# Kernel tuning notes

Hardware: AMD Instinct MI355X
Metric: run time of the kernel (lower is better)

## Reference

```python
import jax, jax.numpy as jnp
import numpy as np

N, K, DIM = 50000, 16, 256
SLOPE = 0.2

def _leaky(x):
    return jnp.where(x >= 0, x, SLOPE * x)

def _mlp(x, w, b):
    # torch nn.Linear followed by LeakyReLU(0.2); w is [in, out]
    return _leaky(x @ w + b)

def setup_inputs() -> dict:
    key = jax.random.key(0)
    ks = jax.random.split(key, 14)
    d4, d2 = DIM // 4, DIM // 2
    def lin(k, i, o):
        kw, kb = jax.random.split(k)
        s = 1.0 / np.sqrt(i)
        return (jax.random.uniform(kw, (i, o), jnp.float32, -s, s),
                jax.random.uniform(kb, (o,), jnp.float32, -s, s))
    w_res, b_res = lin(ks[0], DIM, DIM)
    w_init, b_init = lin(ks[1], DIM, d4)
    w_g1, b_g1 = lin(ks[2], 4, d4)
    w_g2, b_g2 = lin(ks[3], 4, d2)
    w_fin, b_fin = lin(ks[4], DIM, DIM)
    return {
        "input_features": jax.random.normal(ks[5], (N, DIM), jnp.float32),
        "geom_features": jax.random.normal(ks[6], (N, K, 4), jnp.float32),
        "closest_indices": jax.random.randint(ks[7], (N, K), 0, N, jnp.int32),
        "w_res": w_res, "b_res": b_res,
        "w_init": w_init, "b_init": b_init,
        "w_g1": w_g1, "b_g1": b_g1,
        "w_g2": w_g2, "b_g2": b_g2,
        "w_fin": w_fin, "b_fin": b_fin,
    }

def _lfa(feat, geom, idx, w_g, b_g):
    # feat: [N, d]; geom: [N, K, 4]; idx: [N, K]
    g = _mlp(geom, w_g, b_g)                 # [N, K, d]
    gathered = feat[idx]                      # [N, K, d] gather over points
    combined = jnp.concatenate([g, gathered], axis=-1)  # [N, K, 2d]
    return jnp.mean(combined, axis=1)         # [N, 2d]

def reference(input_features, geom_features, closest_indices,
              w_res, b_res, w_init, b_init, w_g1, b_g1, w_g2, b_g2,
              w_fin, b_fin):
    residual = _mlp(input_features, w_res, b_res)            # [N, DIM]
    a = _mlp(input_features, w_init, b_init)                 # [N, DIM/4]
    a = _lfa(a, geom_features, closest_indices, w_g1, b_g1)  # [N, DIM/2]
    a = _lfa(a, geom_features, closest_indices, w_g2, b_g2)  # [N, DIM]
    a = _mlp(a, w_fin, b_fin)                                # [N, DIM]
    return a + residual
```

## Files before the change

### kernel.cpp

```cpp
#include <hip/hip_runtime.h>

#define DIM 256
#define KNN 16
#define SLOPE 0.2f

typedef unsigned short u16;
typedef __attribute__((ext_vector_type(8))) unsigned short u16x8;
typedef __attribute__((ext_vector_type(4))) unsigned short u16x4;
typedef __attribute__((ext_vector_type(8))) short s16x8;
typedef __attribute__((ext_vector_type(4))) float f32x4;

__device__ __forceinline__ float leaky(float x) { return x >= 0.f ? x : SLOPE * x; }
__device__ __forceinline__ u16 f2bu(float f) {
    unsigned int u = __float_as_uint(f);
    u = (u + 0x7FFFu + ((u >> 16) & 1u)) >> 16;
    return (u16)u;
}
__device__ __forceinline__ float bu2f(u16 h) {
    return __uint_as_float(((unsigned int)h) << 16);
}

__global__ __launch_bounds__(256) void k_prep(
    const float* __restrict__ w_res, const float* __restrict__ w_init,
    const float* __restrict__ w_fin, u16* __restrict__ wT1, u16* __restrict__ wT3)
{
    const int t = blockIdx.x * 256 + threadIdx.x;
    if (t < 20 * 8 * 64) {
        const int lane = t & 63, frag = t >> 6;
        const int ks = frag & 7, ct = frag >> 3;
        const int col = ct * 16 + (lane & 15);
        const int k0 = ks * 32 + (lane >> 4) * 8;
        u16x8 p;
        #pragma unroll
        for (int j = 0; j < 8; ++j) {
            float v = (col < 256) ? w_res[(size_t)(k0 + j) * 256 + col]
                                  : w_init[(size_t)(k0 + j) * 64 + (col - 256)];
            p[j] = f2bu(v);
        }
        *(u16x8*)(wT1 + (size_t)t * 8) = p;
    } else if (t < 20 * 8 * 64 + 16 * 8 * 64) {
        const int u = t - 20 * 8 * 64;
        const int lane = u & 63, frag = u >> 6;
        const int ks = frag & 7, ct = frag >> 3;
        const int col = ct * 16 + (lane & 15);
        const int k0 = ks * 32 + (lane >> 4) * 8;
        u16x8 p;
        #pragma unroll
        for (int j = 0; j < 8; ++j)
            p[j] = f2bu(w_fin[(size_t)(k0 + j) * 256 + col]);
        *(u16x8*)(wT3 + (size_t)u * 8) = p;
    }
}

#define APAD 264
__global__ __launch_bounds__(256) void k_gemm1(
    const float* __restrict__ in, const u16* __restrict__ wT1,
    const float* __restrict__ b_res, const float* __restrict__ b_init,
    float* __restrict__ resid, u16* __restrict__ a1, int N)
{
    __shared__ u16 A_s[64 * APAD];
    const int t = threadIdx.x;
    const int base = blockIdx.x * 64;

    {
        const int row = t >> 2, seg = t & 3;
        const int grow = min(base + row, N - 1);
        const float* src = in + (size_t)grow * DIM + seg * 64;
        u16* dst = &A_s[row * APAD + seg * 64];
        #pragma unroll
        for (int j = 0; j < 8; ++j) {
            float4 f0 = *(const float4*)(src + j * 8);
            float4 f1 = *(const float4*)(src + j * 8 + 4);
            u16x8 p;
            p[0] = f2bu(f0.x); p[1] = f2bu(f0.y); p[2] = f2bu(f0.z); p[3] = f2bu(f0.w);
            p[4] = f2bu(f1.x); p[5] = f2bu(f1.y); p[6] = f2bu(f1.z); p[7] = f2bu(f1.w);
            *(u16x8*)(dst + j * 8) = p;
        }
    }
    __syncthreads();

    f32x4 acc[4][5];
    #pragma unroll
    for (int i = 0; i < 4; ++i)
        #pragma unroll
        for (int j = 0; j < 5; ++j)
            acc[i][j] = (f32x4){0.f, 0.f, 0.f, 0.f};

    const int w = t >> 6, lane = t & 63;
    const int llow = lane & 15, lhi = lane >> 4;

    for (int ks = 0; ks < 8; ++ks) {
        s16x8 bfrag[5];
        #pragma unroll
        for (int ci = 0; ci < 5; ++ci) {
            const int ct = w * 5 + ci;
            bfrag[ci] = *(const s16x8*)(wT1 + ((size_t)(ct * 8 + ks) * 64 + lane) * 8);
        }
        s16x8 afrag[4];
        #pragma unroll
        for (int rt = 0; rt < 4; ++rt)
            afrag[rt] = *(const s16x8*)(&A_s[(rt * 16 + llow) * APAD + ks * 32 + lhi * 8]);
        #pragma unroll
        for (int ci = 0; ci < 5; ++ci)
            #pragma unroll
            for (int rt = 0; rt < 4; ++rt)
                acc[rt][ci] = __builtin_amdgcn_mfma_f32_16x16x32_bf16(
                    afrag[rt], bfrag[ci], acc[rt][ci], 0, 0, 0);
    }

    #pragma unroll
    for (int ci = 0; ci < 5; ++ci) {
        const int ct = w * 5 + ci;
        const int col = ct * 16 + llow;
        if (col < 256) {
            const float bias = b_res[col];
            #pragma unroll
            for (int rt = 0; rt < 4; ++rt)
                #pragma unroll
                for (int r = 0; r < 4; ++r) {
                    int row = base + rt * 16 + lhi * 4 + r;
                    if (row < N)
                        resid[(size_t)row * DIM + col] = leaky(acc[rt][ci][r] + bias);
                }
        } else {
            const int c2 = col - 256;
            const float bias = b_init[c2];
            #pragma unroll
            for (int rt = 0; rt < 4; ++rt)
                #pragma unroll
                for (int r = 0; r < 4; ++r) {
                    int row = base + rt * 16 + lhi * 4 + r;
                    if (row < N)
                        a1[(size_t)row * 64 + c2] = f2bu(leaky(acc[rt][ci][r] + bias));
                }
        }
    }
}

__global__ __launch_bounds__(256) void k_lfa1(
    const float* __restrict__ geom, const int* __restrict__ idx,
    const float* __restrict__ w_g1, const float* __restrict__ b_g1,
    const u16* __restrict__ a1, u16* __restrict__ a2, int N)
{
    __shared__ float geom_s[16 * KNN * 4];
    __shared__ int idx_s[16 * KNN];
    const int t = threadIdx.x;
    const int base = blockIdx.x * 16;

    {
        size_t off = (size_t)base * 64 + t * 4;
        size_t mx = (size_t)N * 64 - 4;
        if (off > mx) off = mx;
        *(float4*)&geom_s[t * 4] = *(const float4*)(geom + off);
        int io = base * KNN + t;
        if (t < 256) idx_s[t] = idx[min(io, N * KNN - 1)];
    }
    __syncthreads();

    const int pt = t >> 4, s = t & 15;
    const int n = base + pt;

    float wr[4][4], bb[4];
    #pragma unroll
    for (int r = 0; r < 4; ++r)
        #pragma unroll
        for (int j = 0; j < 4; ++j)
            wr[r][j] = w_g1[r * 64 + s * 4 + j];
    #pragma unroll
    for (int j = 0; j < 4; ++j) bb[j] = b_g1[s * 4 + j];

    float accM[4] = {0.f, 0.f, 0.f, 0.f};
    const float4* g4 = (const float4*)&geom_s[pt * 64];
    #pragma unroll
    for (int k = 0; k < KNN; ++k) {
        float4 g = g4[k];
        #pragma unroll
        for (int j = 0; j < 4; ++j)
            accM[j] += leaky(g.x * wr[0][j] + g.y * wr[1][j] + g.z * wr[2][j] + g.w * wr[3][j] + bb[j]);
    }

    float accG[4] = {0.f, 0.f, 0.f, 0.f};
    #pragma unroll
    for (int k = 0; k < KNN; ++k) {
        u16x4 u = *(const u16x4*)(a1 + (size_t)idx_s[pt * KNN + k] * 64 + s * 4);
        #pragma unroll
        for (int j = 0; j < 4; ++j) accG[j] += bu2f(u[j]);
    }

    if (n < N) {
        u16x4 pm, pg;
        #pragma unroll
        for (int j = 0; j < 4; ++j) {
            pm[j] = f2bu(accM[j] * 0.0625f);
            pg[j] = f2bu(accG[j] * 0.0625f);
        }
        *(u16x4*)(a2 + (size_t)n * 128 + s * 4) = pm;
        *(u16x4*)(a2 + (size_t)n * 128 + 64 + s * 4) = pg;
    }
}

__global__ __launch_bounds__(256) void k_lfa2_fin(
    const float* __restrict__ geom, const int* __restrict__ idx,
    const float* __restrict__ w_g2, const float* __restrict__ b_g2,
    const u16* __restrict__ a2, const u16* __restrict__ wT3,
    const float* __restrict__ b_fin, float* __restrict__ out, int N)
{
    __shared__ u16 a3_s[64 * APAD];
    __shared__ float geom_s[64 * KNN * 4];
    __shared__ int idx_s[64 * KNN];
    const int t = threadIdx.x;
    const int base = blockIdx.x * 64;

    {
        size_t mx = (size_t)N * 64 - 4;
        #pragma unroll
        for (int j = 0; j < 4; ++j) {
            size_t off = (size_t)base * 64 + t * 4 + j * 1024;
            if (off > mx) off = mx;
            *(float4*)&geom_s[t * 4 + j * 1024] = *(const float4*)(geom + off);
        }
        int imx = N * KNN - 1;
        #pragma unroll
        for (int j = 0; j < 4; ++j) {
            int off = base * KNN + t + j * 256;
            idx_s[t + j * 256] = idx[min(off, imx)];
        }
    }
    __syncthreads();

    {
        const int c = t & 127, h = t >> 7;
        const float w0 = w_g2[c], w1 = w_g2[128 + c], w2 = w_g2[256 + c],
                    w3 = w_g2[384 + c], bb = b_g2[c];
        for (int p = 0; p < 32; ++p) {
            const int pt = h * 32 + p;
            float acc = 0.f;
            const float4* g4 = (const float4*)&geom_s[pt * 64];
            #pragma unroll
            for (int k = 0; k < KNN; ++k) {
                float4 g = g4[k];
                acc += leaky(g.x * w0 + g.y * w1 + g.z * w2 + g.w * w3 + bb);
            }
            a3_s[pt * APAD + c] = f2bu(acc * 0.0625f);
        }
    }
    {
        const int pt = t >> 2, q = t & 3;
        float acc[32];
        #pragma unroll
        for (int j = 0; j < 32; ++j) acc[j] = 0.f;
        for (int k = 0; k < KNN; ++k) {
            const u16* row = a2 + (size_t)idx_s[pt * KNN + k] * 128 + q * 32;
            #pragma unroll
            for (int v = 0; v < 4; ++v) {
                u16x8 u = *(const u16x8*)(row + v * 8);
                #pragma unroll
                for (int j = 0; j < 8; ++j) acc[v * 8 + j] += bu2f(u[j]);
            }
        }
        #pragma unroll
        for (int v = 0; v < 4; ++v) {
            u16x8 p;
            #pragma unroll
            for (int j = 0; j < 8; ++j) p[j] = f2bu(acc[v * 8 + j] * 0.0625f);
            *(u16x8*)(&a3_s[pt * APAD + 128 + q * 32 + v * 8]) = p;
        }
    }
    __syncthreads();

    f32x4 acc[4][4];
    #pragma unroll
    for (int i = 0; i < 4; ++i)
        #pragma unroll
        for (int j = 0; j < 4; ++j)
            acc[i][j] = (f32x4){0.f, 0.f, 0.f, 0.f};

    const int w = t >> 6, lane = t & 63;
    const int llow = lane & 15, lhi = lane >> 4;

    for (int ks = 0; ks < 8; ++ks) {
        s16x8 bfrag[4];
        #pragma unroll
        for (int ci = 0; ci < 4; ++ci) {
            const int ct = w * 4 + ci;
            bfrag[ci] = *(const s16x8*)(wT3 + ((size_t)(ct * 8 + ks) * 64 + lane) * 8);
        }
        s16x8 afrag[4];
        #pragma unroll
        for (int rt = 0; rt < 4; ++rt)
            afrag[rt] = *(const s16x8*)(&a3_s[(rt * 16 + llow) * APAD + ks * 32 + lhi * 8]);
        #pragma unroll
        for (int ci = 0; ci < 4; ++ci)
            #pragma unroll
            for (int rt = 0; rt < 4; ++rt)
                acc[rt][ci] = __builtin_amdgcn_mfma_f32_16x16x32_bf16(
                    afrag[rt], bfrag[ci], acc[rt][ci], 0, 0, 0);
    }

    #pragma unroll
    for (int ci = 0; ci < 4; ++ci) {
        const int ct = w * 4 + ci;
        const int col = ct * 16 + llow;
        const float bias = b_fin[col];
        #pragma unroll
        for (int rt = 0; rt < 4; ++rt)
            #pragma unroll
            for (int r = 0; r < 4; ++r) {
                int row = base + rt * 16 + lhi * 4 + r;
                if (row < N) {
                    size_t o = (size_t)row * DIM + col;
                    out[o] = leaky(acc[rt][ci][r] + bias) + out[o];
                }
            }
    }
}

extern "C" void kernel_launch(void* const* d_in, const int* in_sizes, int n_in,
                              void* d_out, int out_size, void* d_ws, size_t ws_size,
                              hipStream_t stream) {
    const float* in    = (const float*)d_in[0];
    const float* geom  = (const float*)d_in[1];
    const int*   idx   = (const int*)d_in[2];
    const float* w_res = (const float*)d_in[3];
    const float* b_res = (const float*)d_in[4];
    const float* w_init= (const float*)d_in[5];
    const float* b_init= (const float*)d_in[6];
    const float* w_g1  = (const float*)d_in[7];
    const float* b_g1  = (const float*)d_in[8];
    const float* w_g2  = (const float*)d_in[9];
    const float* b_g2  = (const float*)d_in[10];
    const float* w_fin = (const float*)d_in[11];
    const float* b_fin = (const float*)d_in[12];
    float* out = (float*)d_out;

    const int N = in_sizes[0] / DIM;

    char* ws = (char*)d_ws;
    u16* a1  = (u16*)ws;
    u16* a2  = (u16*)(ws + (size_t)N * 64 * 2);
    u16* wT1 = (u16*)(ws + (size_t)N * (64 + 128) * 2);
    u16* wT3 = wT1 + 320 * 256;

    k_prep<<<72, 256, 0, stream>>>(w_res, w_init, w_fin, wT1, wT3);
    k_gemm1<<<(N + 63) / 64, 256, 0, stream>>>(in, wT1, b_res, b_init, out, a1, N);
    k_lfa1<<<(N + 15) / 16, 256, 0, stream>>>(geom, idx, w_g1, b_g1, a1, a2, N);
    k_lfa2_fin<<<(N + 63) / 64, 256, 0, stream>>>(geom, idx, w_g2, b_g2, a2, wT3, b_fin, out, N);
}
```

Before: 296.9 us.

## Split gemm1 accumulators into two passes and drop LDS staging in lfa2_fin

k_gemm1 now computes its five column tiles in two passes (3 then 2) with a shared epilogue helper, which shrinks the live accumulator set so that launch_bounds(256,4) can fit. k_lfa2_fin drops the geom and idx shared-memory staging and its barrier, reading geom directly from global memory and loading each point's indices as int4 vectors. Its gather loop now issues two neighbours' loads before accumulating, to keep more memory requests in flight. In exchange, the A fragments are reloaded from LDS in both gemm1 passes, and the geom reads in lfa2_fin are redundant across threads and may hit global or L2 repeatedly.

```diff
diff --git a/kernel.cpp b/kernel.cpp
--- a/kernel.cpp
+++ b/kernel.cpp
@@ -53,7 +53,38 @@
 }
 
 #define APAD 264
-__global__ __launch_bounds__(256) void k_gemm1(
+
+__device__ __forceinline__ void epi_gemm1(
+    int base, int N, int ct, int llow, int lhi, const f32x4* acc4,
+    const float* __restrict__ b_res, const float* __restrict__ b_init,
+    float* __restrict__ resid, u16* __restrict__ a1)
+{
+    const int col = ct * 16 + llow;
+    if (col < 256) {
+        const float bias = b_res[col];
+        #pragma unroll
+        for (int rt = 0; rt < 4; ++rt)
+            #pragma unroll
+            for (int r = 0; r < 4; ++r) {
+                int row = base + rt * 16 + lhi * 4 + r;
+                if (row < N)
+                    resid[(size_t)row * DIM + col] = leaky(acc4[rt][r] + bias);
+            }
+    } else {
+        const int c2 = col - 256;
+        const float bias = b_init[c2];
+        #pragma unroll
+        for (int rt = 0; rt < 4; ++rt)
+            #pragma unroll
+            for (int r = 0; r < 4; ++r) {
+                int row = base + rt * 16 + lhi * 4 + r;
+                if (row < N)
+                    a1[(size_t)row * 64 + c2] = f2bu(leaky(acc4[rt][r] + bias));
+            }
+    }
+}
+
+__global__ __launch_bounds__(256, 4) void k_gemm1(
     const float* __restrict__ in, const u16* __restrict__ wT1,
     const float* __restrict__ b_res, const float* __restrict__ b_init,
     float* __restrict__ resid, u16* __restrict__ a1, int N)
@@ -79,61 +110,66 @@
     }
     __syncthreads();
 
-    f32x4 acc[4][5];
-    #pragma unroll
-    for (int i = 0; i < 4; ++i)
-        #pragma unroll
-        for (int j = 0; j < 5; ++j)
-            acc[i][j] = (f32x4){0.f, 0.f, 0.f, 0.f};
-
     const int w = t >> 6, lane = t & 63;
     const int llow = lane & 15, lhi = lane >> 4;
 
-    for (int ks = 0; ks < 8; ++ks) {
-        s16x8 bfrag[5];
-        #pragma unroll
-        for (int ci = 0; ci < 5; ++ci) {
-            const int ct = w * 5 + ci;
-            bfrag[ci] = *(const s16x8*)(wT1 + ((size_t)(ct * 8 + ks) * 64 + lane) * 8);
-        }
-        s16x8 afrag[4];
-        #pragma unroll
-        for (int rt = 0; rt < 4; ++rt)
-            afrag[rt] = *(const s16x8*)(&A_s[(rt * 16 + llow) * APAD + ks * 32 + lhi * 8]);
-        #pragma unroll
-        for (int ci = 0; ci < 5; ++ci)
+    {
+        f32x4 acc[3][4];
+        #pragma unroll
+        for (int i = 0; i < 3; ++i)
+            #pragma unroll
+            for (int j = 0; j < 4; ++j)
+                acc[i][j] = (f32x4){0.f, 0.f, 0.f, 0.f};
+        for (int ks = 0; ks < 8; ++ks) {
+            s16x8 bfrag[3];
+            #pragma unroll
+            for (int ci = 0; ci < 3; ++ci) {
+                const int ct = w * 5 + ci;
+                bfrag[ci] = *(const s16x8*)(wT1 + ((size_t)(ct * 8 + ks) * 64 + lane) * 8);
+            }
+            s16x8 afrag[4];
             #pragma unroll
             for (int rt = 0; rt < 4; ++rt)
-                acc[rt][ci] = __builtin_amdgcn_mfma_f32_16x16x32_bf16(
-                    afrag[rt], bfrag[ci], acc[rt][ci], 0, 0, 0);
-    }
-
-    #pragma unroll
-    for (int ci = 0; ci < 5; ++ci) {
-        const int ct = w * 5 + ci;
-        const int col = ct * 16 + llow;
-        if (col < 256) {
-            const float bias = b_res[col];
+                afrag[rt] = *(const s16x8*)(&A_s[(rt * 16 + llow) * APAD + ks * 32 + lhi * 8]);
+            #pragma unroll
+            for (int ci = 0; ci < 3; ++ci)
+                #pragma unroll
+                for (int rt = 0; rt < 4; ++rt)
+                    acc[ci][rt] = __builtin_amdgcn_mfma_f32_16x16x32_bf16(
+                        afrag[rt], bfrag[ci], acc[ci][rt], 0, 0, 0);
+        }
+        #pragma unroll
+        for (int ci = 0; ci < 3; ++ci)
+            epi_gemm1(base, N, w * 5 + ci, llow, lhi, acc[ci], b_res, b_init, resid, a1);
+    }
+    {
+        f32x4 acc[2][4];
+        #pragma unroll
+        for (int i = 0; i < 2; ++i)
+            #pragma unroll
+            for (int j = 0; j < 4; ++j)
+                acc[i][j] = (f32x4){0.f, 0.f, 0.f, 0.f};
+        for (int ks = 0; ks < 8; ++ks) {
+            s16x8 bfrag[2];
+            #pragma unroll
+            for (int ci = 0; ci < 2; ++ci) {
+                const int ct = w * 5 + 3 + ci;
+                bfrag[ci] = *(const s16x8*)(wT1 + ((size_t)(ct * 8 + ks) * 64 + lane) * 8);
+            }
+            s16x8 afrag[4];
             #pragma unroll
             for (int rt = 0; rt < 4; ++rt)
+                afrag[rt] = *(const s16x8*)(&A_s[(rt * 16 + llow) * APAD + ks * 32 + lhi * 8]);
+            #pragma unroll
+            for (int ci = 0; ci < 2; ++ci)
                 #pragma unroll
-                for (int r = 0; r < 4; ++r) {
-                    int row = base + rt * 16 + lhi * 4 + r;
-                    if (row < N)
-                        resid[(size_t)row * DIM + col] = leaky(acc[rt][ci][r] + bias);
-                }
-        } else {
-            const int c2 = col - 256;
-            const float bias = b_init[c2];
-            #pragma unroll
-            for (int rt = 0; rt < 4; ++rt)
-                #pragma unroll
-                for (int r = 0; r < 4; ++r) {
-                    int row = base + rt * 16 + lhi * 4 + r;
-                    if (row < N)
-                        a1[(size_t)row * 64 + c2] = f2bu(leaky(acc[rt][ci][r] + bias));
-                }
-        }
+                for (int rt = 0; rt < 4; ++rt)
+                    acc[ci][rt] = __builtin_amdgcn_mfma_f32_16x16x32_bf16(
+                        afrag[rt], bfrag[ci], acc[ci][rt], 0, 0, 0);
+        }
+        #pragma unroll
+        for (int ci = 0; ci < 2; ++ci)
+            epi_gemm1(base, N, w * 5 + 3 + ci, llow, lhi, acc[ci], b_res, b_init, resid, a1);
     }
 }
 
@@ -199,34 +235,15 @@
     }
 }
 
-__global__ __launch_bounds__(256) void k_lfa2_fin(
+__global__ __launch_bounds__(256, 4) void k_lfa2_fin(
     const float* __restrict__ geom, const int* __restrict__ idx,
     const float* __restrict__ w_g2, const float* __restrict__ b_g2,
     const u16* __restrict__ a2, const u16* __restrict__ wT3,
     const float* __restrict__ b_fin, float* __restrict__ out, int N)
 {
     __shared__ u16 a3_s[64 * APAD];
-    __shared__ float geom_s[64 * KNN * 4];
-    __shared__ int idx_s[64 * KNN];
     const int t = threadIdx.x;
     const int base = blockIdx.x * 64;
-
-    {
-        size_t mx = (size_t)N * 64 - 4;
-        #pragma unroll
-        for (int j = 0; j < 4; ++j) {
-            size_t off = (size_t)base * 64 + t * 4 + j * 1024;
-            if (off > mx) off = mx;
-            *(float4*)&geom_s[t * 4 + j * 1024] = *(const float4*)(geom + off);
-        }
-        int imx = N * KNN - 1;
-        #pragma unroll
-        for (int j = 0; j < 4; ++j) {
-            int off = base * KNN + t + j * 256;
-            idx_s[t + j * 256] = idx[min(off, imx)];
-        }
-    }
-    __syncthreads();
 
     {
         const int c = t & 127, h = t >> 7;
@@ -234,8 +251,9 @@
                     w3 = w_g2[384 + c], bb = b_g2[c];
         for (int p = 0; p < 32; ++p) {
             const int pt = h * 32 + p;
+            const int n = min(base + pt, N - 1);
+            const float4* g4 = (const float4*)(geom + (size_t)n * 64);
             float acc = 0.f;
-            const float4* g4 = (const float4*)&geom_s[pt * 64];
             #pragma unroll
             for (int k = 0; k < KNN; ++k) {
                 float4 g = g4[k];
@@ -246,17 +264,33 @@
     }
     {
         const int pt = t >> 2, q = t & 3;
+        const int n = min(base + pt, N - 1);
+        int4 i0 = *(const int4*)(idx + (size_t)n * KNN);
+        int4 i1 = *(const int4*)(idx + (size_t)n * KNN + 4);
+        int4 i2 = *(const int4*)(idx + (size_t)n * KNN + 8);
+        int4 i3 = *(const int4*)(idx + (size_t)n * KNN + 12);
+        const int ind[16] = {i0.x, i0.y, i0.z, i0.w, i1.x, i1.y, i1.z, i1.w,
+                             i2.x, i2.y, i2.z, i2.w, i3.x, i3.y, i3.z, i3.w};
         float acc[32];
         #pragma unroll
         for (int j = 0; j < 32; ++j) acc[j] = 0.f;
-        for (int k = 0; k < KNN; ++k) {
-            const u16* row = a2 + (size_t)idx_s[pt * KNN + k] * 128 + q * 32;
-            #pragma unroll
-            for (int v = 0; v < 4; ++v) {
-                u16x8 u = *(const u16x8*)(row + v * 8);
+        #pragma unroll
+        for (int kb = 0; kb < 8; ++kb) {
+            u16x8 u[2][4];
+            #pragma unroll
+            for (int h2 = 0; h2 < 2; ++h2) {
+                const u16* row = a2 + (size_t)ind[kb * 2 + h2] * 128 + q * 32;
                 #pragma unroll
-                for (int j = 0; j < 8; ++j) acc[v * 8 + j] += bu2f(u[j]);
-            }
+                for (int v = 0; v < 4; ++v)
+                    u[h2][v] = *(const u16x8*)(row + v * 8);
+            }
+            #pragma unroll
+            for (int h2 = 0; h2 < 2; ++h2)
+                #pragma unroll
+                for (int v = 0; v < 4; ++v)
+                    #pragma unroll
+                    for (int j = 0; j < 8; ++j)
+                        acc[v * 8 + j] += bu2f(u[h2][v][j]);
         }
         #pragma unroll
         for (int v = 0; v < 4; ++v) {
```

Result: slower. 349.6 us (+17.8%).

## Split fused LFA2+final GEMM into a gather kernel and a separate MFMA GEMM kernel

Applied to the files above, without the earlier changes.

When the workspace is large enough, the fused LFA2+final-linear kernel is replaced by two kernels. A gather kernel uses four threads per point with wide bf16 row loads and computes the geometry MLP mean from a transposed w_g2. A separate MFMA GEMM kernel then reads the bf16 intermediate a3 and adds the residual. The aim is higher occupancy and better gather memory parallelism than the shared-memory-bound fused kernel, at the cost of an extra N×256 bf16 round trip through global memory and one more launch; the fused kernel is kept as a fallback.

```diff
diff --git a/kernel.cpp b/kernel.cpp
--- a/kernel.cpp
+++ b/kernel.cpp
@@ -22,7 +22,9 @@
 
 __global__ __launch_bounds__(256) void k_prep(
     const float* __restrict__ w_res, const float* __restrict__ w_init,
-    const float* __restrict__ w_fin, u16* __restrict__ wT1, u16* __restrict__ wT3)
+    const float* __restrict__ w_fin, const float* __restrict__ w_g2,
+    u16* __restrict__ wT1, u16* __restrict__ wT3, float* __restrict__ w_g2T,
+    int do_t)
 {
     const int t = blockIdx.x * 256 + threadIdx.x;
     if (t < 20 * 8 * 64) {
@@ -49,10 +51,16 @@
         for (int j = 0; j < 8; ++j)
             p[j] = f2bu(w_fin[(size_t)(k0 + j) * 256 + col]);
         *(u16x8*)(wT3 + (size_t)u * 8) = p;
+    } else if (do_t && t < 20 * 8 * 64 + 16 * 8 * 64 + 128) {
+        const int o = t - (20 * 8 * 64 + 16 * 8 * 64);
+        float4 v;
+        v.x = w_g2[o]; v.y = w_g2[128 + o]; v.z = w_g2[256 + o]; v.w = w_g2[384 + o];
+        *(float4*)(w_g2T + (size_t)o * 4) = v;
     }
 }
 
 #define APAD 264
+
 __global__ __launch_bounds__(256) void k_gemm1(
     const float* __restrict__ in, const u16* __restrict__ wT1,
     const float* __restrict__ b_res, const float* __restrict__ b_init,
@@ -199,7 +207,143 @@
     }
 }
 
-__global__ __launch_bounds__(256) void k_lfa2_fin(
+__global__ __launch_bounds__(256, 4) void k_gather2(
+    const float* __restrict__ geom, const int* __restrict__ idx,
+    const float* __restrict__ w_g2T, const float* __restrict__ b_g2,
+    const u16* __restrict__ a2, u16* __restrict__ a3, int N)
+{
+    const int t = blockIdx.x * 256 + threadIdx.x;
+    const int pt = t >> 2, q = t & 3;
+    if (pt >= N) return;
+
+    {
+        int4 i0 = *(const int4*)(idx + (size_t)pt * KNN);
+        int4 i1 = *(const int4*)(idx + (size_t)pt * KNN + 4);
+        int4 i2 = *(const int4*)(idx + (size_t)pt * KNN + 8);
+        int4 i3 = *(const int4*)(idx + (size_t)pt * KNN + 12);
+        const int ind[16] = {i0.x, i0.y, i0.z, i0.w, i1.x, i1.y, i1.z, i1.w,
+                             i2.x, i2.y, i2.z, i2.w, i3.x, i3.y, i3.z, i3.w};
+        float acc[32];
+        #pragma unroll
+        for (int j = 0; j < 32; ++j) acc[j] = 0.f;
+        #pragma unroll
+        for (int kb = 0; kb < 8; ++kb) {
+            u16x8 u[2][4];
+            #pragma unroll
+            for (int h2 = 0; h2 < 2; ++h2) {
+                const u16* row = a2 + (size_t)ind[kb * 2 + h2] * 128 + q * 32;
+                #pragma unroll
+                for (int v = 0; v < 4; ++v)
+                    u[h2][v] = *(const u16x8*)(row + v * 8);
+            }
+            #pragma unroll
+            for (int h2 = 0; h2 < 2; ++h2)
+                #pragma unroll
+                for (int v = 0; v < 4; ++v)
+                    #pragma unroll
+                    for (int j = 0; j < 8; ++j)
+                        acc[v * 8 + j] += bu2f(u[h2][v][j]);
+        }
+        #pragma unroll
+        for (int v = 0; v < 4; ++v) {
+            u16x8 p;
+            #pragma unroll
+            for (int j = 0; j < 8; ++j) p[j] = f2bu(acc[v * 8 + j] * 0.0625f);
+            *(u16x8*)(a3 + (size_t)pt * 256 + 128 + q * 32 + v * 8) = p;
+        }
+    }
+
+    {
+        float4 g[KNN];
+        const float4* gp = (const float4*)(geom + (size_t)pt * 64);
+        #pragma unroll
+        for (int k = 0; k < KNN; ++k) g[k] = gp[k];
+        #pragma unroll
+        for (int v = 0; v < 4; ++v) {
+            u16x8 p;
+            #pragma unroll
+            for (int j = 0; j < 8; ++j) {
+                const int c = q * 32 + v * 8 + j;
+                float4 wv = *(const float4*)(w_g2T + (size_t)c * 4);
+                const float bb = b_g2[c];
+                float s = 0.f;
+                #pragma unroll
+                for (int k = 0; k < KNN; ++k)
+                    s += leaky(g[k].x * wv.x + g[k].y * wv.y + g[k].z * wv.z + g[k].w * wv.w + bb);
+                p[j] = f2bu(s * 0.0625f);
+            }
+            *(u16x8*)(a3 + (size_t)pt * 256 + q * 32 + v * 8) = p;
+        }
+    }
+}
+
+__global__ __launch_bounds__(256) void k_fin(
+    const u16* __restrict__ a3, const u16* __restrict__ wT3,
+    const float* __restrict__ b_fin, float* __restrict__ out, int N)
+{
+    __shared__ u16 A_s[64 * APAD];
+    const int t = threadIdx.x;
+    const int base = blockIdx.x * 64;
+
+    {
+        const int row = t >> 2, seg = t & 3;
+        const int grow = min(base + row, N - 1);
+        const u16* src = a3 + (size_t)grow * 256 + seg * 64;
+        u16* dst = &A_s[row * APAD + seg * 64];
+        #pragma unroll
+        for (int j = 0; j < 8; ++j)
+            *(u16x8*)(dst + j * 8) = *(const u16x8*)(src + j * 8);
+    }
+    __syncthreads();
+
+    f32x4 acc[4][4];
+    #pragma unroll
+    for (int i = 0; i < 4; ++i)
+        #pragma unroll
+        for (int j = 0; j < 4; ++j)
+            acc[i][j] = (f32x4){0.f, 0.f, 0.f, 0.f};
+
+    const int w = t >> 6, lane = t & 63;
+    const int llow = lane & 15, lhi = lane >> 4;
+
+    for (int ks = 0; ks < 8; ++ks) {
+        s16x8 bfrag[4];
+        #pragma unroll
+        for (int ci = 0; ci < 4; ++ci) {
+            const int ct = w * 4 + ci;
+            bfrag[ci] = *(const s16x8*)(wT3 + ((size_t)(ct * 8 + ks) * 64 + lane) * 8);
+        }
+        s16x8 afrag[4];
+        #pragma unroll
+        for (int rt = 0; rt < 4; ++rt)
+            afrag[rt] = *(const s16x8*)(&A_s[(rt * 16 + llow) * APAD + ks * 32 + lhi * 8]);
+        #pragma unroll
+        for (int ci = 0; ci < 4; ++ci)
+            #pragma unroll
+            for (int rt = 0; rt < 4; ++rt)
+                acc[rt][ci] = __builtin_amdgcn_mfma_f32_16x16x32_bf16(
+                    afrag[rt], bfrag[ci], acc[rt][ci], 0, 0, 0);
+    }
+
+    #pragma unroll
+    for (int ci = 0; ci < 4; ++ci) {
+        const int ct = w * 4 + ci;
+        const int col = ct * 16 + llow;
+        const float bias = b_fin[col];
+        #pragma unroll
+        for (int rt = 0; rt < 4; ++rt)
+            #pragma unroll
+            for (int r = 0; r < 4; ++r) {
+                int row = base + rt * 16 + lhi * 4 + r;
+                if (row < N) {
+                    size_t o = (size_t)row * DIM + col;
+                    out[o] = leaky(acc[rt][ci][r] + bias) + out[o];
+                }
+            }
+    }
+}
+
+__global__ __launch_bounds__(256) void k_lfa2_fin_fused(
     const float* __restrict__ geom, const int* __restrict__ idx,
     const float* __restrict__ w_g2, const float* __restrict__ b_g2,
     const u16* __restrict__ a2, const u16* __restrict__ wT3,
@@ -335,14 +479,26 @@
 
     const int N = in_sizes[0] / DIM;
 
+    const size_t need = (size_t)N * (64 + 128 + 256) * 2
+                        + 320 * 256 * 2 + 256 * 256 * 2 + 128 * 4 * 4;
+    const bool split = ws_size >= need;
+
     char* ws = (char*)d_ws;
-    u16* a1  = (u16*)ws;
-    u16* a2  = (u16*)(ws + (size_t)N * 64 * 2);
-    u16* wT1 = (u16*)(ws + (size_t)N * (64 + 128) * 2);
+    u16* a1 = (u16*)ws;
+    u16* a2 = a1 + (size_t)N * 64;
+    u16* a3 = a2 + (size_t)N * 128;
+    u16* wT1 = split ? (a3 + (size_t)N * 256) : (a2 + (size_t)N * 128);
     u16* wT3 = wT1 + 320 * 256;
-
-    k_prep<<<72, 256, 0, stream>>>(w_res, w_init, w_fin, wT1, wT3);
+    float* w_g2T = (float*)(wT3 + 256 * 256);
+
+    k_prep<<<73, 256, 0, stream>>>(w_res, w_init, w_fin, w_g2, wT1, wT3,
+                                   w_g2T, split ? 1 : 0);
     k_gemm1<<<(N + 63) / 64, 256, 0, stream>>>(in, wT1, b_res, b_init, out, a1, N);
     k_lfa1<<<(N + 15) / 16, 256, 0, stream>>>(geom, idx, w_g1, b_g1, a1, a2, N);
-    k_lfa2_fin<<<(N + 63) / 64, 256, 0, stream>>>(geom, idx, w_g2, b_g2, a2, wT3, b_fin, out, N);
-}
+    if (split) {
+        k_gather2<<<(N * 4 + 255) / 256, 256, 0, stream>>>(geom, idx, w_g2T, b_g2, a2, a3, N);
+        k_fin<<<(N + 63) / 64, 256, 0, stream>>>(a3, wT3, b_fin, out, N);
+    } else {
+        k_lfa2_fin_fused<<<(N + 63) / 64, 256, 0, stream>>>(geom, idx, w_g2, b_g2, a2, wT3, b_fin, out, N);
+    }
+}
```

After: 514.2 us. 73.2% more time.

## Move residual GEMM into final kernel to avoid residual round-trip through output

Applied to the files above, without the earlier changes.

The residual linear layer is no longer computed in the first GEMM kernel, which now produces only the 64-wide init projection. The final kernel reloads the input rows, converts them to bf16 in shared memory after the fin GEMM, runs the residual GEMM, and writes out fin+residual in one store. This removes the fp32 residual write and later read-modify-write of the output (about 100MB of traffic). In exchange the input is read twice, the final kernel holds more registers for the kept fin results, and it gains an extra shared-memory pass and sync.

```diff
diff --git a/kernel.cpp b/kernel.cpp
--- a/kernel.cpp
+++ b/kernel.cpp
@@ -53,10 +53,10 @@
 }
 
 #define APAD 264
-__global__ __launch_bounds__(256) void k_gemm1(
+
+__global__ __launch_bounds__(256) void k_gemm1a(
     const float* __restrict__ in, const u16* __restrict__ wT1,
-    const float* __restrict__ b_res, const float* __restrict__ b_init,
-    float* __restrict__ resid, u16* __restrict__ a1, int N)
+    const float* __restrict__ b_init, u16* __restrict__ a1, int N)
 {
     __shared__ u16 A_s[64 * APAD];
     const int t = threadIdx.x;
@@ -79,62 +79,35 @@
     }
     __syncthreads();
 
-    f32x4 acc[4][5];
-    #pragma unroll
-    for (int i = 0; i < 4; ++i)
-        #pragma unroll
-        for (int j = 0; j < 5; ++j)
-            acc[i][j] = (f32x4){0.f, 0.f, 0.f, 0.f};
-
     const int w = t >> 6, lane = t & 63;
     const int llow = lane & 15, lhi = lane >> 4;
+    const int ct = 16 + w;
+
+    f32x4 acc[4];
+    #pragma unroll
+    for (int i = 0; i < 4; ++i) acc[i] = (f32x4){0.f, 0.f, 0.f, 0.f};
 
     for (int ks = 0; ks < 8; ++ks) {
-        s16x8 bfrag[5];
-        #pragma unroll
-        for (int ci = 0; ci < 5; ++ci) {
-            const int ct = w * 5 + ci;
-            bfrag[ci] = *(const s16x8*)(wT1 + ((size_t)(ct * 8 + ks) * 64 + lane) * 8);
-        }
+        s16x8 bfrag = *(const s16x8*)(wT1 + ((size_t)(ct * 8 + ks) * 64 + lane) * 8);
         s16x8 afrag[4];
         #pragma unroll
         for (int rt = 0; rt < 4; ++rt)
             afrag[rt] = *(const s16x8*)(&A_s[(rt * 16 + llow) * APAD + ks * 32 + lhi * 8]);
         #pragma unroll
-        for (int ci = 0; ci < 5; ++ci)
-            #pragma unroll
-            for (int rt = 0; rt < 4; ++rt)
-                acc[rt][ci] = __builtin_amdgcn_mfma_f32_16x16x32_bf16(
-                    afrag[rt], bfrag[ci], acc[rt][ci], 0, 0, 0);
-    }
-
-    #pragma unroll
-    for (int ci = 0; ci < 5; ++ci) {
-        const int ct = w * 5 + ci;
-        const int col = ct * 16 + llow;
-        if (col < 256) {
-            const float bias = b_res[col];
-            #pragma unroll
-            for (int rt = 0; rt < 4; ++rt)
-                #pragma unroll
-                for (int r = 0; r < 4; ++r) {
-                    int row = base + rt * 16 + lhi * 4 + r;
-                    if (row < N)
-                        resid[(size_t)row * DIM + col] = leaky(acc[rt][ci][r] + bias);
-                }
-        } else {
-            const int c2 = col - 256;
-            const float bias = b_init[c2];
-            #pragma unroll
-            for (int rt = 0; rt < 4; ++rt)
-                #pragma unroll
-                for (int r = 0; r < 4; ++r) {
-                    int row = base + rt * 16 + lhi * 4 + r;
-                    if (row < N)
-                        a1[(size_t)row * 64 + c2] = f2bu(leaky(acc[rt][ci][r] + bias));
-                }
-        }
-    }
+        for (int rt = 0; rt < 4; ++rt)
+            acc[rt] = __builtin_amdgcn_mfma_f32_16x16x32_bf16(afrag[rt], bfrag, acc[rt], 0, 0, 0);
+    }
+
+    const int c2 = w * 16 + llow;
+    const float bias = b_init[c2];
+    #pragma unroll
+    for (int rt = 0; rt < 4; ++rt)
+        #pragma unroll
+        for (int r = 0; r < 4; ++r) {
+            int row = base + rt * 16 + lhi * 4 + r;
+            if (row < N)
+                a1[(size_t)row * 64 + c2] = f2bu(leaky(acc[rt][r] + bias));
+        }
 }
 
 __global__ __launch_bounds__(256) void k_lfa1(
@@ -200,9 +173,11 @@
 }
 
 __global__ __launch_bounds__(256) void k_lfa2_fin(
-    const float* __restrict__ geom, const int* __restrict__ idx,
+    const float* __restrict__ in, const float* __restrict__ geom,
+    const int* __restrict__ idx,
     const float* __restrict__ w_g2, const float* __restrict__ b_g2,
-    const u16* __restrict__ a2, const u16* __restrict__ wT3,
+    const u16* __restrict__ a2, const u16* __restrict__ wT1,
+    const u16* __restrict__ wT3, const float* __restrict__ b_res,
     const float* __restrict__ b_fin, float* __restrict__ out, int N)
 {
     __shared__ u16 a3_s[64 * APAD];
@@ -268,22 +243,78 @@
     }
     __syncthreads();
 
-    f32x4 acc[4][4];
-    #pragma unroll
-    for (int i = 0; i < 4; ++i)
-        #pragma unroll
-        for (int j = 0; j < 4; ++j)
-            acc[i][j] = (f32x4){0.f, 0.f, 0.f, 0.f};
-
     const int w = t >> 6, lane = t & 63;
     const int llow = lane & 15, lhi = lane >> 4;
 
+    f32x4 o[4][4];
+    {
+        f32x4 acc[4][4];
+        #pragma unroll
+        for (int i = 0; i < 4; ++i)
+            #pragma unroll
+            for (int j = 0; j < 4; ++j)
+                acc[i][j] = (f32x4){0.f, 0.f, 0.f, 0.f};
+
+        for (int ks = 0; ks < 8; ++ks) {
+            s16x8 bfrag[4];
+            #pragma unroll
+            for (int ci = 0; ci < 4; ++ci) {
+                const int ct = w * 4 + ci;
+                bfrag[ci] = *(const s16x8*)(wT3 + ((size_t)(ct * 8 + ks) * 64 + lane) * 8);
+            }
+            s16x8 afrag[4];
+            #pragma unroll
+            for (int rt = 0; rt < 4; ++rt)
+                afrag[rt] = *(const s16x8*)(&a3_s[(rt * 16 + llow) * APAD + ks * 32 + lhi * 8]);
+            #pragma unroll
+            for (int ci = 0; ci < 4; ++ci)
+                #pragma unroll
+                for (int rt = 0; rt < 4; ++rt)
+                    acc[rt][ci] = __builtin_amdgcn_mfma_f32_16x16x32_bf16(
+                        afrag[rt], bfrag[ci], acc[rt][ci], 0, 0, 0);
+        }
+        #pragma unroll
+        for (int ci = 0; ci < 4; ++ci) {
+            const float bias = b_fin[(w * 4 + ci) * 16 + llow];
+            #pragma unroll
+            for (int rt = 0; rt < 4; ++rt)
+                #pragma unroll
+                for (int r = 0; r < 4; ++r)
+                    o[rt][ci][r] = leaky(acc[rt][ci][r] + bias);
+        }
+    }
+    __syncthreads();
+
+    {
+        const int row = t >> 2, seg = t & 3;
+        const int grow = min(base + row, N - 1);
+        const float* src = in + (size_t)grow * DIM + seg * 64;
+        u16* dst = &a3_s[row * APAD + seg * 64];
+        #pragma unroll
+        for (int j = 0; j < 8; ++j) {
+            float4 f0 = *(const float4*)(src + j * 8);
+            float4 f1 = *(const float4*)(src + j * 8 + 4);
+            u16x8 p;
+            p[0] = f2bu(f0.x); p[1] = f2bu(f0.y); p[2] = f2bu(f0.z); p[3] = f2bu(f0.w);
+            p[4] = f2bu(f1.x); p[5] = f2bu(f1.y); p[6] = f2bu(f1.z); p[7] = f2bu(f1.w);
+            *(u16x8*)(dst + j * 8) = p;
+        }
+    }
+    __syncthreads();
+
+    f32x4 acc2[4][4];
+    #pragma unroll
+    for (int i = 0; i < 4; ++i)
+        #pragma unroll
+        for (int j = 0; j < 4; ++j)
+            acc2[i][j] = (f32x4){0.f, 0.f, 0.f, 0.f};
+
     for (int ks = 0; ks < 8; ++ks) {
         s16x8 bfrag[4];
         #pragma unroll
         for (int ci = 0; ci < 4; ++ci) {
             const int ct = w * 4 + ci;
-            bfrag[ci] = *(const s16x8*)(wT3 + ((size_t)(ct * 8 + ks) * 64 + lane) * 8);
+            bfrag[ci] = *(const s16x8*)(wT1 + ((size_t)(ct * 8 + ks) * 64 + lane) * 8);
         }
         s16x8 afrag[4];
         #pragma unroll
@@ -293,24 +324,21 @@
         for (int ci = 0; ci < 4; ++ci)
             #pragma unroll
             for (int rt = 0; rt < 4; ++rt)
-                acc[rt][ci] = __builtin_amdgcn_mfma_f32_16x16x32_bf16(
-                    afrag[rt], bfrag[ci], acc[rt][ci], 0, 0, 0);
+                acc2[rt][ci] = __builtin_amdgcn_mfma_f32_16x16x32_bf16(
+                    afrag[rt], bfrag[ci], acc2[rt][ci], 0, 0, 0);
     }
 
     #pragma unroll
     for (int ci = 0; ci < 4; ++ci) {
-        const int ct = w * 4 + ci;
-        const int col = ct * 16 + llow;
-        const float bias = b_fin[col];
+        const int col = (w * 4 + ci) * 16 + llow;
+        const float bias = b_res[col];
         #pragma unroll
         for (int rt = 0; rt < 4; ++rt)
             #pragma unroll
             for (int r = 0; r < 4; ++r) {
                 int row = base + rt * 16 + lhi * 4 + r;
-                if (row < N) {
-                    size_t o = (size_t)row * DIM + col;
-                    out[o] = leaky(acc[rt][ci][r] + bias) + out[o];
-                }
+                if (row < N)
+                    out[(size_t)row * DIM + col] = o[rt][ci][r] + leaky(acc2[rt][ci][r] + bias);
             }
     }
 }
@@ -337,12 +365,13 @@
 
     char* ws = (char*)d_ws;
     u16* a1  = (u16*)ws;
-    u16* a2  = (u16*)(ws + (size_t)N * 64 * 2);
-    u16* wT1 = (u16*)(ws + (size_t)N * (64 + 128) * 2);
+    u16* a2  = a1 + (size_t)N * 64;
+    u16* wT1 = a2 + (size_t)N * 128;
     u16* wT3 = wT1 + 320 * 256;
 
     k_prep<<<72, 256, 0, stream>>>(w_res, w_init, w_fin, wT1, wT3);
-    k_gemm1<<<(N + 63) / 64, 256, 0, stream>>>(in, wT1, b_res, b_init, out, a1, N);
+    k_gemm1a<<<(N + 63) / 64, 256, 0, stream>>>(in, wT1, b_init, a1, N);
     k_lfa1<<<(N + 15) / 16, 256, 0, stream>>>(geom, idx, w_g1, b_g1, a1, a2, N);
-    k_lfa2_fin<<<(N + 63) / 64, 256, 0, stream>>>(geom, idx, w_g2, b_g2, a2, wT3, b_fin, out, N);
-}
+    k_lfa2_fin<<<(N + 63) / 64, 256, 0, stream>>>(in, geom, idx, w_g2, b_g2, a2,
+                                                  wT1, wT3, b_res, b_fin, out, N);
+}
```

Result: slower. 306.9 us (+3.3%).
